# Kernel tuning notes

Measured on AMD Instinct MI355X. Metric: run time of the kernel, lower is better.

Reference implementation:

```python
import jax, jax.numpy as jnp
import numpy as np

B, L, D = 4, 1024, 256
HD = 16                 # head_dim
H = D // HD             # num heads = 16
DI = 2 * D              # mamba d_inner (expand=2) = 512
S = 64                  # d_state
KC = 4                  # d_conv
DTR = max(1, D // 16)   # dt_rank = 16
SCALES = (1, 2, 4, 8)


def _lin_interp(x, L_out):
    # F.interpolate(mode='linear', align_corners=False) on (B, L_in, D)
    L_in = x.shape[1]
    pos = (jnp.arange(L_out, dtype=x.dtype) + 0.5) * (L_in / L_out) - 0.5
    pos = jnp.clip(pos, 0.0, L_in - 1)
    lo = jnp.floor(pos).astype(jnp.int32)
    hi = jnp.minimum(lo + 1, L_in - 1)
    w = (pos - lo.astype(x.dtype))[None, :, None]
    return x[:, lo] * (1.0 - w) + x[:, hi] * w


def setup_inputs() -> dict:
    key = jax.random.key(0)
    ks = jax.random.split(key, 24)
    sc = 0.02
    inp = {
        "x": jax.random.normal(ks[0], (B, L, D), jnp.float32),
        "ln_g": jnp.ones((D,), jnp.float32),
        "ln_b": jnp.zeros((D,), jnp.float32),
        # MultiScaleQuery: 4 per-scale projections + fuse
        "mq_w": sc * jax.random.normal(ks[1], (4, D, D), jnp.float32),
        "mq_b": sc * jax.random.normal(ks[2], (4, D), jnp.float32),
        "fuse_w": sc * jax.random.normal(ks[3], (D, 4 * D), jnp.float32),
        "fuse_b": sc * jax.random.normal(ks[4], (D,), jnp.float32),
        # Mamba params
        "in_proj_w": sc * jax.random.normal(ks[5], (2 * DI, D), jnp.float32),
        "conv_w": 0.2 * jax.random.normal(ks[6], (DI, KC), jnp.float32),
        "conv_b": sc * jax.random.normal(ks[7], (DI,), jnp.float32),
        "x_proj_w": sc * jax.random.normal(ks[8], (DTR + 2 * S, DI), jnp.float32),
        "dt_w": sc * jax.random.normal(ks[9], (DI, DTR), jnp.float32),
        "dt_b": jnp.full((DI,), -4.0, jnp.float32),  # softplus -> small dt
        "A_log": jnp.log(jnp.tile(jnp.arange(1, S + 1, dtype=jnp.float32), (DI, 1))),
        "D_ssm": jnp.ones((DI,), jnp.float32),
        "out_w": sc * jax.random.normal(ks[10], (D, DI), jnp.float32),
        # StructuredSSD (q comes from MultiScaleQuery override; q_proj unused)
        "k_w": sc * jax.random.normal(ks[11], (D, D), jnp.float32),
        "k_b": sc * jax.random.normal(ks[12], (D,), jnp.float32),
        "v_w": sc * jax.random.normal(ks[13], (D, D), jnp.float32),
        "v_b": sc * jax.random.normal(ks[14], (D,), jnp.float32),
        "o_w": sc * jax.random.normal(ks[15], (D, D), jnp.float32),
        "o_b": sc * jax.random.normal(ks[16], (D,), jnp.float32),
        "log_tau": jnp.full((H,), np.log(16.0), jnp.float32),
        # Gate
        "gate_w": sc * jax.random.normal(ks[17], (D, 2 * D), jnp.float32),
        "gate_b": sc * jax.random.normal(ks[18], (D,), jnp.float32),
    }
    return inp


def reference(x, ln_g, ln_b, mq_w, mq_b, fuse_w, fuse_b,
              in_proj_w, conv_w, conv_b, x_proj_w, dt_w, dt_b,
              A_log, D_ssm, out_w,
              k_w, k_b, v_w, v_b, o_w, o_b, log_tau,
              gate_w, gate_b):
    Bsz, Lq, Dm = x.shape

    # ---- LayerNorm ----
    mu = x.mean(-1, keepdims=True)
    var = ((x - mu) ** 2).mean(-1, keepdims=True)
    xn = (x - mu) / jnp.sqrt(var + 1e-5) * ln_g + ln_b

    # ---- MultiScaleQuery ----
    qs = []
    for i, s in enumerate(SCALES):
        if s <= 1:
            q = xn @ mq_w[i].T + mq_b[i]
        else:
            xd = xn.reshape(Bsz, Lq // s, s, Dm).mean(2)   # avg_pool1d(k=s, stride=s)
            qd = xd @ mq_w[i].T + mq_b[i]
            q = _lin_interp(qd, Lq)
        qs.append(q)
    q = jnp.concatenate(qs, -1) @ fuse_w.T + fuse_b        # (B, L, D)

    # ---- Mamba (selective scan) ----
    xz = xn @ in_proj_w.T                                  # (B, L, 2*DI)
    xm, z = jnp.split(xz, 2, axis=-1)
    xp = jnp.pad(xm, ((0, 0), (KC - 1, 0), (0, 0)))        # causal depthwise conv
    xc = sum(xp[:, kk:kk + Lq, :] * conv_w[:, kk] for kk in range(KC)) + conv_b
    xc = jax.nn.silu(xc)                                   # (B, L, DI)
    dbc = xc @ x_proj_w.T                                  # (B, L, DTR+2S)
    dt_in, Bm, Cm = jnp.split(dbc, [DTR, DTR + S], axis=-1)
    dt = jax.nn.softplus(dt_in @ dt_w.T + dt_b)            # (B, L, DI)
    A = -jnp.exp(A_log)                                    # (DI, S)

    def step(h, inp):
        xt, dtt, Bt, Ct = inp                              # (B,DI) (B,DI) (B,S) (B,S)
        dA = jnp.exp(dtt[:, :, None] * A)                  # (B, DI, S)
        h = dA * h + (dtt * xt)[:, :, None] * Bt[:, None, :]
        y = jnp.einsum('bds,bs->bd', h, Ct)
        return h, y

    h0 = jnp.zeros((Bsz, DI, S), x.dtype)
    _, ys = jax.lax.scan(step, h0, (xc.transpose(1, 0, 2), dt.transpose(1, 0, 2),
                                    Bm.transpose(1, 0, 2), Cm.transpose(1, 0, 2)))
    y = ys.transpose(1, 0, 2) + xc * D_ssm                 # (B, L, DI)
    y = y * jax.nn.silu(z)
    ssm_out = y @ out_w.T                                  # (B, L, D)

    # ---- StructuredSSD (decay-masked attention, q override) ----
    k = xn @ k_w.T + k_b
    v = xn @ v_w.T + v_b
    hds = lambda t: t.reshape(Bsz, Lq, H, HD).transpose(0, 2, 1, 3)
    qh, kh, vh = hds(q), hds(k), hds(v)                    # (B, H, L, hd)
    scale = 1.0 / np.sqrt(HD)
    scores = jnp.einsum('bhqd,bhkd->bhqk', qh, kh) * scale
    idx = jnp.arange(Lq)
    dist = jnp.maximum(idx[:, None] - idx[None, :], 0).astype(x.dtype)
    tau = jnp.exp(log_tau)[:, None, None]                  # (H,1,1)
    mask = jnp.exp(-dist / tau)                            # (H, L, L); ==1 above diag
    scores = scores * mask
    denom = jnp.maximum(mask.sum(-1, keepdims=True), 1e-6)
    scores = scores / denom                                # broadcast over batch
    attn = jnp.einsum('bhqk,bhkd->bhqd', scores, vh)
    attn = attn.transpose(0, 2, 1, 3).reshape(Bsz, Lq, Dm)
    ssd_out = attn @ o_w.T + o_b

    # ---- Sigmoid gate fusion + residual ----
    gate = jax.nn.sigmoid(jnp.concatenate([ssm_out, ssd_out], -1) @ gate_w.T + gate_b)
    fused = gate * ssm_out + (1.0 - gate) * ssd_out
    return x + fused
```

## Files before the change

### kernel.cpp

```cpp
#include <hip/hip_runtime.h>
#include <math.h>

#define Bsz 4
#define Lseq 1024
#define Dm 256
#define Hh 16
#define HDm 16
#define DIm 512
#define Ssz 64
#define KCm 4
#define DTRm 16
#define NCH (Bsz * DIm)
#define CHK 64
#define NCHK (Lseq / CHK)
#define CHA 16
#define NCA (Lseq / CHA)

typedef __attribute__((ext_vector_type(8))) short s8v;
typedef __attribute__((ext_vector_type(4))) float f4v;

static __device__ __forceinline__ float wave_sum(float v) {
    #pragma unroll
    for (int m = 32; m >= 1; m >>= 1) v += __shfl_xor(v, m, 64);
    return v;
}

static __device__ __forceinline__ float bcast(float v, int l) {
    return __uint_as_float(__builtin_amdgcn_readlane(__float_as_uint(v), l));
}

static __device__ __forceinline__ short f2bf(float f) {
    unsigned int u = __float_as_uint(f);
    u = (u + 0x7fffu + ((u >> 16) & 1u)) >> 16;
    return (short)u;
}

static __device__ __forceinline__ s8v pack8(float4 a, float4 b) {
    s8v v;
    v[0] = f2bf(a.x); v[1] = f2bf(a.y); v[2] = f2bf(a.z); v[3] = f2bf(a.w);
    v[4] = f2bf(b.x); v[5] = f2bf(b.y); v[6] = f2bf(b.z); v[7] = f2bf(b.w);
    return v;
}

__global__ __launch_bounds__(256) void ln_pool(const float* __restrict__ x,
                                               const float* __restrict__ g,
                                               const float* __restrict__ bb,
                                               float* __restrict__ xn, float* __restrict__ xd2,
                                               float* __restrict__ xd4, float* __restrict__ xd8) {
    __shared__ float p2[4][256];
    int wid = threadIdx.x >> 6, lane = threadIdx.x & 63;
    int gr0 = blockIdx.x * 8;
    int b = gr0 >> 10, t0 = gr0 & 1023;
    float4 g4 = *(const float4*)(g + lane * 4);
    float4 b4 = *(const float4*)(bb + lane * 4);
    float4 res[2];
    #pragma unroll
    for (int rr = 0; rr < 2; rr++) {
        int row = gr0 + wid * 2 + rr;
        float4 xv = *(const float4*)(x + (size_t)row * 256 + lane * 4);
        float s = wave_sum(xv.x + xv.y + xv.z + xv.w);
        float mean = s * (1.0f / 256.0f);
        float d0 = xv.x - mean, d1 = xv.y - mean, d2 = xv.z - mean, d3 = xv.w - mean;
        float s2 = wave_sum(d0 * d0 + d1 * d1 + d2 * d2 + d3 * d3);
        float inv = rsqrtf(s2 * (1.0f / 256.0f) + 1e-5f);
        float4 r;
        r.x = d0 * inv * g4.x + b4.x; r.y = d1 * inv * g4.y + b4.y;
        r.z = d2 * inv * g4.z + b4.z; r.w = d3 * inv * g4.w + b4.w;
        *(float4*)(xn + (size_t)row * 256 + lane * 4) = r;
        res[rr] = r;
    }
    float4 a2;
    a2.x = 0.5f * (res[0].x + res[1].x); a2.y = 0.5f * (res[0].y + res[1].y);
    a2.z = 0.5f * (res[0].z + res[1].z); a2.w = 0.5f * (res[0].w + res[1].w);
    *(float4*)(xd2 + (size_t)(b * 512 + (t0 >> 1) + wid) * 256 + lane * 4) = a2;
    *(float4*)&p2[wid][lane * 4] = a2;
    __syncthreads();
    if (wid < 2) {
        float4 u = *(const float4*)&p2[2 * wid][lane * 4];
        float4 w = *(const float4*)&p2[2 * wid + 1][lane * 4];
        float4 m;
        m.x = 0.5f * (u.x + w.x); m.y = 0.5f * (u.y + w.y);
        m.z = 0.5f * (u.z + w.z); m.w = 0.5f * (u.w + w.w);
        *(float4*)(xd4 + (size_t)(b * 256 + (t0 >> 2) + wid) * 256 + lane * 4) = m;
    } else if (wid == 2) {
        float4 q0 = *(const float4*)&p2[0][lane * 4];
        float4 q1 = *(const float4*)&p2[1][lane * 4];
        float4 q2 = *(const float4*)&p2[2][lane * 4];
        float4 q3 = *(const float4*)&p2[3][lane * 4];
        float4 m;
        m.x = 0.25f * ((q0.x + q1.x) + (q2.x + q3.x));
        m.y = 0.25f * ((q0.y + q1.y) + (q2.y + q3.y));
        m.z = 0.25f * ((q0.z + q1.z) + (q2.z + q3.z));
        m.w = 0.25f * ((q0.w + q1.w) + (q2.w + q3.w));
        *(float4*)(xd8 + (size_t)(b * 128 + (t0 >> 3)) * 256 + lane * 4) = m;
    }
}

__global__ __launch_bounds__(256) void proj8(const float* __restrict__ xn,
                                             const float* __restrict__ xd2,
                                             const float* __restrict__ xd4,
                                             const float* __restrict__ xd8,
                                             const float* __restrict__ in_proj_w,
                                             const float* __restrict__ k_w, const float* __restrict__ k_b,
                                             const float* __restrict__ v_w, const float* __restrict__ v_b,
                                             const float* __restrict__ mq_w, const float* __restrict__ mq_b,
                                             float* __restrict__ xm, float* __restrict__ zT,
                                             float* __restrict__ kmat, float* __restrict__ vmat,
                                             float* __restrict__ q0, float* __restrict__ qd2,
                                             float* __restrict__ qd4, float* __restrict__ qd8) {
    __shared__ unsigned short As[64][40];
    __shared__ unsigned short Ws[64][40];
    int bx = blockIdx.x;
    const float* A; const float* W; const float* bias; float* C;
    int ldc, transC = 0, n0, m0;
    if (bx < 512) {
        A = xn; W = in_proj_w; bias = nullptr; C = xm; ldc = DIm;
        n0 = (bx & 7) * 64; m0 = (bx >> 3) * 64;
    } else if (bx < 1024) {
        int l = bx - 512;
        A = xn; W = in_proj_w + 131072; bias = nullptr; C = zT; ldc = Bsz * Lseq; transC = 1;
        n0 = (l & 7) * 64; m0 = (l >> 3) * 64;
    } else if (bx < 1280) {
        int l = bx - 1024;
        A = xn; W = k_w; bias = k_b; C = kmat; ldc = Dm;
        n0 = (l & 3) * 64; m0 = (l >> 2) * 64;
    } else if (bx < 1536) {
        int l = bx - 1280;
        A = xn; W = v_w; bias = v_b; C = vmat; ldc = Dm;
        n0 = (l & 3) * 64; m0 = (l >> 2) * 64;
    } else if (bx < 1792) {
        int l = bx - 1536;
        A = xn; W = mq_w; bias = mq_b; C = q0; ldc = Dm;
        n0 = (l & 3) * 64; m0 = (l >> 2) * 64;
    } else if (bx < 1920) {
        int l = bx - 1792;
        A = xd2; W = mq_w + 65536; bias = mq_b + 256; C = qd2; ldc = Dm;
        n0 = (l & 3) * 64; m0 = (l >> 2) * 64;
    } else if (bx < 1984) {
        int l = bx - 1920;
        A = xd4; W = mq_w + 131072; bias = mq_b + 512; C = qd4; ldc = Dm;
        n0 = (l & 3) * 64; m0 = (l >> 2) * 64;
    } else {
        int l = bx - 1984;
        A = xd8; W = mq_w + 196608; bias = mq_b + 768; C = qd8; ldc = Dm;
        n0 = (l & 3) * 64; m0 = (l >> 2) * 64;
    }
    int tid = threadIdx.x;
    int wave = tid >> 6, lane = tid & 63;
    int quad = lane >> 4, r = lane & 15;
    int mo = (wave >> 1) * 32, no = (wave & 1) * 32;
    f4v acc[2][2];
    #pragma unroll
    for (int i = 0; i < 2; i++)
        #pragma unroll
        for (int j = 0; j < 2; j++) acc[i][j] = (f4v){0.f, 0.f, 0.f, 0.f};
    for (int k0 = 0; k0 < 256; k0 += 32) {
        {
            int m = tid >> 2, kk = (tid & 3) * 8;
            const float* ap = A + (size_t)(m0 + m) * 256 + k0 + kk;
            *(s8v*)&As[m][kk] = pack8(*(const float4*)ap, *(const float4*)(ap + 4));
        }
        {
            int n = tid >> 2, kk = (tid & 3) * 8;
            const float* wp = W + (size_t)(n0 + n) * 256 + k0 + kk;
            *(s8v*)&Ws[n][kk] = pack8(*(const float4*)wp, *(const float4*)(wp + 4));
        }
        __syncthreads();
        s8v af[2], bf[2];
        #pragma unroll
        for (int i = 0; i < 2; i++) af[i] = *(const s8v*)&As[mo + i * 16 + r][quad * 8];
        #pragma unroll
        for (int j = 0; j < 2; j++) bf[j] = *(const s8v*)&Ws[no + j * 16 + r][quad * 8];
        #pragma unroll
        for (int i = 0; i < 2; i++)
            #pragma unroll
            for (int j = 0; j < 2; j++)
                acc[i][j] = __builtin_amdgcn_mfma_f32_16x16x32_bf16(af[i], bf[j], acc[i][j], 0, 0, 0);
        __syncthreads();
    }
    #pragma unroll
    for (int i = 0; i < 2; i++)
        #pragma unroll
        for (int j = 0; j < 2; j++)
            #pragma unroll
            for (int reg = 0; reg < 4; reg++) {
                int m = m0 + mo + i * 16 + quad * 4 + reg;
                int n = n0 + no + j * 16 + r;
                float v = acc[i][j][reg];
                if (bias) v += bias[n];
                float* cp = transC ? (C + (size_t)n * ldc + m) : (C + (size_t)m * ldc + n);
                *cp = v;
            }
}

__global__ __launch_bounds__(256) void mid2(const float* __restrict__ q0,
                                            const float* __restrict__ qd2,
                                            const float* __restrict__ qd4,
                                            const float* __restrict__ qd8,
                                            const float* __restrict__ fuse_w,
                                            const float* __restrict__ fuse_b,
                                            float* __restrict__ qbuf,
                                            const float* __restrict__ xm,
                                            const float* __restrict__ cw,
                                            const float* __restrict__ cb,
                                            float* __restrict__ xc, float* __restrict__ xcT) {
    __shared__ __align__(16) char smem[16640];
    int bx = blockIdx.x;
    int tid = threadIdx.x;
    if (bx < 256) {
        unsigned short (*As)[40] = (unsigned short(*)[40])smem;
        unsigned short (*Ws)[40] = (unsigned short(*)[40])(smem + 5120);
        int wave = tid >> 6, lane = tid & 63;
        int quad = lane >> 4, r = lane & 15;
        int n0 = (bx & 3) * 64, m0 = (bx >> 2) * 64;
        int mo = (wave >> 1) * 32, no = (wave & 1) * 32;
        f4v acc[2][2];
        #pragma unroll
        for (int i = 0; i < 2; i++)
            #pragma unroll
            for (int j = 0; j < 2; j++) acc[i][j] = (f4v){0.f, 0.f, 0.f, 0.f};
        for (int k0 = 0; k0 < 1024; k0 += 32) {
            {
                int m = tid >> 2, kk = (tid & 3) * 8;
                int kg = k0 + kk;
                int seg = kg >> 8, dcol = kg & 255;
                int mg = m0 + m;
                s8v pv;
                if (seg == 0) {
                    const float* ap = q0 + (size_t)mg * 256 + dcol;
                    pv = pack8(*(const float4*)ap, *(const float4*)(ap + 4));
                } else {
                    int t = mg & 1023, b = mg >> 10;
                    int Lin = 512 >> (seg - 1);
                    const float* qd = (seg == 1) ? qd2 : (seg == 2) ? qd4 : qd8;
                    float pos = (t + 0.5f) * ((float)Lin / 1024.0f) - 0.5f;
                    pos = fminf(fmaxf(pos, 0.0f), (float)(Lin - 1));
                    int lo = (int)floorf(pos);
                    int hi = min(lo + 1, Lin - 1);
                    float w = pos - (float)lo;
                    const float* plo = qd + ((size_t)(b * Lin + lo)) * 256 + dcol;
                    const float* phi = qd + ((size_t)(b * Lin + hi)) * 256 + dcol;
                    float4 l0 = *(const float4*)plo, l1 = *(const float4*)(plo + 4);
                    float4 h0 = *(const float4*)phi, h1 = *(const float4*)(phi + 4);
                    float4 r0, r1;
                    r0.x = l0.x + w * (h0.x - l0.x); r0.y = l0.y + w * (h0.y - l0.y);
                    r0.z = l0.z + w * (h0.z - l0.z); r0.w = l0.w + w * (h0.w - l0.w);
                    r1.x = l1.x + w * (h1.x - l1.x); r1.y = l1.y + w * (h1.y - l1.y);
                    r1.z = l1.z + w * (h1.z - l1.z); r1.w = l1.w + w * (h1.w - l1.w);
                    pv = pack8(r0, r1);
                }
                *(s8v*)&As[m][kk] = pv;
            }
            {
                int n = tid >> 2, kk = (tid & 3) * 8;
                const float* wp = fuse_w + (size_t)(n0 + n) * 1024 + k0 + kk;
                *(s8v*)&Ws[n][kk] = pack8(*(const float4*)wp, *(const float4*)(wp + 4));
            }
            __syncthreads();
            s8v af[2], bf[2];
            #pragma unroll
            for (int i = 0; i < 2; i++) af[i] = *(const s8v*)&As[mo + i * 16 + r][quad * 8];
            #pragma unroll
            for (int j = 0; j < 2; j++) bf[j] = *(const s8v*)&Ws[no + j * 16 + r][quad * 8];
            #pragma unroll
            for (int i = 0; i < 2; i++)
                #pragma unroll
                for (int j = 0; j < 2; j++)
                    acc[i][j] = __builtin_amdgcn_mfma_f32_16x16x32_bf16(af[i], bf[j], acc[i][j], 0, 0, 0);
            __syncthreads();
        }
        #pragma unroll
        for (int i = 0; i < 2; i++)
            #pragma unroll
            for (int j = 0; j < 2; j++)
                #pragma unroll
                for (int reg = 0; reg < 4; reg++) {
                    int m = m0 + mo + i * 16 + quad * 4 + reg;
                    int n = n0 + no + j * 16 + r;
                    qbuf[(size_t)m * 256 + n] = acc[i][j][reg] + fuse_b[n];
                }
    } else {
        float (*tile)[65] = (float(*)[65])smem;
        int blk = bx - 256;
        int cblk = blk & 7;
        int tblk = (blk >> 3) & 15;
        int b = blk >> 7;
        int c0 = cblk * 64, t0 = tblk * 64;
        int cc = tid & 63;
        int tw = tid >> 6;
        int c = c0 + cc;
        float w0 = cw[c * 4 + 0], w1 = cw[c * 4 + 1], w2 = cw[c * 4 + 2], w3 = cw[c * 4 + 3];
        float bias = cb[c];
        #pragma unroll 4
        for (int i = 0; i < 16; i++) {
            int tl = tw * 16 + i;
            int t = t0 + tl;
            const float* base = xm + ((size_t)(b * Lseq + t)) * DIm + c;
            float acc = bias + base[0] * w3;
            if (t >= 3) {
                acc += base[-3 * DIm] * w0 + base[-2 * DIm] * w1 + base[-1 * DIm] * w2;
            } else {
                if (t >= 1) acc += base[-1 * DIm] * w2;
                if (t >= 2) acc += base[-2 * DIm] * w1;
            }
            float r = acc / (1.0f + __expf(-acc));
            xc[((size_t)(b * Lseq + t)) * DIm + c] = r;
            tile[tl][cc] = r;
        }
        __syncthreads();
        int tcol = tid & 63;
        int crow0 = tid >> 6;
        #pragma unroll 4
        for (int j = 0; j < 16; j++) {
            int crow = crow0 * 16 + j;
            xcT[((size_t)(c0 + crow)) * (Bsz * Lseq) + b * Lseq + t0 + tcol] = tile[tcol][crow];
        }
    }
}

__global__ __launch_bounds__(256) void xproj_ap1(const float* __restrict__ xc,
                                                 const float* __restrict__ x_proj_w,
                                                 float* __restrict__ dbc,
                                                 const float* __restrict__ kmat,
                                                 const float* __restrict__ vmat,
                                                 const float* __restrict__ log_tau,
                                                 float* __restrict__ loc) {
    __shared__ __align__(16) char smem[10240];
    int bx = blockIdx.x;
    int tid = threadIdx.x;
    int wid = tid >> 6, lane = tid & 63;
    if (bx < 192) {
        unsigned short (*As)[40] = (unsigned short(*)[40])smem;
        unsigned short (*Ws)[40] = (unsigned short(*)[40])(smem + 5120);
        int quad = lane >> 4, r = lane & 15;
        int n0 = (bx % 3) * 64, m0 = (bx / 3) * 64;
        int mo = (wid >> 1) * 32, no = (wid & 1) * 32;
        f4v acc[2][2];
        #pragma unroll
        for (int i = 0; i < 2; i++)
            #pragma unroll
            for (int j = 0; j < 2; j++) acc[i][j] = (f4v){0.f, 0.f, 0.f, 0.f};
        for (int k0 = 0; k0 < 512; k0 += 32) {
            {
                int m = tid >> 2, kk = (tid & 3) * 8;
                const float* ap = xc + (size_t)(m0 + m) * 512 + k0 + kk;
                *(s8v*)&As[m][kk] = pack8(*(const float4*)ap, *(const float4*)(ap + 4));
            }
            {
                int n = tid >> 2, kk = (tid & 3) * 8;
                s8v pv;
                if (n0 + n < 144) {
                    const float* wp = x_proj_w + (size_t)(n0 + n) * 512 + k0 + kk;
                    pv = pack8(*(const float4*)wp, *(const float4*)(wp + 4));
                } else {
                    pv = (s8v){0, 0, 0, 0, 0, 0, 0, 0};
                }
                *(s8v*)&Ws[n][kk] = pv;
            }
            __syncthreads();
            s8v af[2], bf[2];
            #pragma unroll
            for (int i = 0; i < 2; i++) af[i] = *(const s8v*)&As[mo + i * 16 + r][quad * 8];
            #pragma unroll
            for (int j = 0; j < 2; j++) bf[j] = *(const s8v*)&Ws[no + j * 16 + r][quad * 8];
            #pragma unroll
            for (int i = 0; i < 2; i++)
                #pragma unroll
                for (int j = 0; j < 2; j++)
                    acc[i][j] = __builtin_amdgcn_mfma_f32_16x16x32_bf16(af[i], bf[j], acc[i][j], 0, 0, 0);
            __syncthreads();
        }
        #pragma unroll
        for (int i = 0; i < 2; i++)
            #pragma unroll
            for (int j = 0; j < 2; j++)
                #pragma unroll
                for (int reg = 0; reg < 4; reg++) {
                    int m = m0 + mo + i * 16 + quad * 4 + reg;
                    int n = n0 + no + j * 16 + r;
                    if (n >= 144) continue;
                    dbc[(size_t)m * 144 + n] = acc[i][j][reg];
                }
    } else {
        float (*Ksh)[CHA][20] = (float(*)[CHA][20])smem;
        float (*Vsh)[CHA][16] = (float(*)[CHA][16])(smem + 5120);
        int wv = (bx - 192) * 4 + wid;
        int bh = wv >> 6, c = wv & 63;
        int b = bh >> 4, h = bh & 15;
        float inv_tau = __expf(-log_tau[h]);
        float rdec = __expf(-inv_tau);
        int t0 = c * CHA;
        int row = lane >> 2, q4 = (lane & 3) * 4;
        const float* kp = kmat + ((size_t)(b * Lseq + t0 + row)) * Dm + h * HDm + q4;
        const float* vp = vmat + ((size_t)(b * Lseq + t0 + row)) * Dm + h * HDm + q4;
        *(float4*)&Ksh[wid][row][q4] = *(const float4*)kp;
        *(float4*)&Vsh[wid][row][q4] = *(const float4*)vp;
        int g = lane >> 4, cc = lane & 15;
        float4 U = {0.f, 0.f, 0.f, 0.f}, T = {0.f, 0.f, 0.f, 0.f};
        #pragma unroll
        for (int s = 0; s < CHA; s++) {
            float4 kf = *(const float4*)&Ksh[wid][s][4 * g];
            float vv = Vsh[wid][s][cc];
            float u0 = kf.x * vv, u1 = kf.y * vv, u2 = kf.z * vv, u3 = kf.w * vv;
            U.x += u0; U.y += u1; U.z += u2; U.w += u3;
            T.x = fmaf(rdec, T.x, u0); T.y = fmaf(rdec, T.y, u1);
            T.z = fmaf(rdec, T.z, u2); T.w = fmaf(rdec, T.w, u3);
        }
        float* op = loc + ((size_t)bh * NCA + c) * 512;
        *(float4*)(op + lane * 4) = U;
        *(float4*)(op + 256 + lane * 4) = T;
    }
}

__global__ __launch_bounds__(256) void dt_ap2(const float* __restrict__ dbc,
                                              const float* __restrict__ dt_w,
                                              const float* __restrict__ dt_b,
                                              float* __restrict__ dtmT,
                                              float* __restrict__ loc,
                                              const float* __restrict__ log_tau,
                                              float* __restrict__ kvtot) {
    __shared__ __align__(16) char smem[9216];
    int bx = blockIdx.x;
    int tid = threadIdx.x;
    if (bx < 512) {
        float (*As)[72] = (float(*)[72])smem;
        float (*Ws)[72] = (float(*)[72])(smem + 4608);
        int m0 = (bx >> 3) * 64, n0 = (bx & 7) * 64;
        int tx = tid & 15, ty = tid >> 4;
        float acc[4][4] = {};
        {
            int ml = tid >> 2, kl = (tid & 3) * 4;
            const float4 av = *(const float4*)(dbc + (size_t)(m0 + ml) * 144 + kl);
            As[kl + 0][ml] = av.x; As[kl + 1][ml] = av.y;
            As[kl + 2][ml] = av.z; As[kl + 3][ml] = av.w;
        }
        {
            int nl = tid >> 2, kl = (tid & 3) * 4;
            float4 wv = *(const float4*)(dt_w + (size_t)(n0 + nl) * 16 + kl);
            Ws[kl + 0][nl] = wv.x; Ws[kl + 1][nl] = wv.y;
            Ws[kl + 2][nl] = wv.z; Ws[kl + 3][nl] = wv.w;
        }
        __syncthreads();
        #pragma unroll
        for (int kk = 0; kk < 16; kk++) {
            float4 av = *(const float4*)&As[kk][ty * 4];
            float4 bv = *(const float4*)&Ws[kk][tx * 4];
            float a[4] = {av.x, av.y, av.z, av.w};
            float bbv[4] = {bv.x, bv.y, bv.z, bv.w};
            #pragma unroll
            for (int im = 0; im < 4; im++)
                #pragma unroll
                for (int in = 0; in < 4; in++)
                    acc[im][in] = fmaf(a[im], bbv[in], acc[im][in]);
        }
        #pragma unroll
        for (int in = 0; in < 4; in++) {
            int n = n0 + tx * 4 + in;
            #pragma unroll
            for (int im = 0; im < 4; im++) {
                int m = m0 + ty * 4 + im;
                float v = acc[im][in] + dt_b[n];
                v = fmaxf(v, 0.0f) + log1pf(expf(-fabsf(v)));
                dtmT[(size_t)n * (Bsz * Lseq) + m] = v;
            }
        }
    } else {
        int bh = bx - 512, e = tid;
        float inv_tau = __expf(-log_tau[bh & 15]);
        float rp = __expf(-(float)CHA * inv_tau);
        float* lp = loc + (size_t)bh * NCA * 512;
        float Ua = 0.f, Ta = 0.f;
        #pragma unroll 8
        for (int c = 0; c < NCA; c++) {
            float tu = lp[c * 512 + e];
            lp[c * 512 + e] = Ua;
            Ua += tu;
            float tt = lp[c * 512 + 256 + e];
            lp[c * 512 + 256 + e] = Ta;
            Ta = fmaf(rp, Ta, tt);
        }
        kvtot[bh * 256 + e] = Ua;
    }
}

__global__ __launch_bounds__(256) void sp1_ap3(const float* __restrict__ xcT,
                                               const float* __restrict__ dtmT,
                                               const float* __restrict__ dbc,
                                               const float* __restrict__ A_log,
                                               float* __restrict__ hloc,
                                               float* __restrict__ Pc,
                                               const float* __restrict__ q,
                                               const float* __restrict__ kmat,
                                               const float* __restrict__ vmat,
                                               const float* __restrict__ log_tau,
                                               const float* __restrict__ init,
                                               const float* __restrict__ kvtot,
                                               float* __restrict__ attn_out) {
    __shared__ __align__(16) char smem[18432];
    int bx = blockIdx.x;
    int tid = threadIdx.x;
    int wid = tid >> 6, lane = tid & 63;
    if (bx < 8192) {
        int wave = bx * 4 + wid;
        int ch = wave & (NCH - 1);
        int c  = wave >> 11;
        int b = ch >> 9, d = ch & (DIm - 1);
        float As = -__expf(A_log[d * Ssz + lane]);
        int base_m = b * Lseq + c * CHK;
        float dt_vec = dtmT[(size_t)d * (Bsz * Lseq) + base_m + lane];
        float x_vec  = xcT [(size_t)d * (Bsz * Lseq) + base_m + lane];
        float ux = dt_vec * x_vec;
        float S = dt_vec;
        #pragma unroll
        for (int m = 1; m < 64; m <<= 1) {
            float o = __shfl_up(S, m, 64);
            if (lane >= m) S += o;
        }
        float Stot = bcast(S, 63);
        const float* Bp = dbc + (size_t)base_m * 144 + DTRm + lane;
        float h0 = 0.f, h1 = 0.f, h2 = 0.f, h3 = 0.f;
        #pragma unroll 4
        for (int t = 0; t < CHK; t += 4) {
            float B0 = Bp[0], B1 = Bp[144], B2 = Bp[288], B3 = Bp[432];
            Bp += 576;
            float w0 = __expf(As * (Stot - bcast(S, t)))     * bcast(ux, t);
            float w1 = __expf(As * (Stot - bcast(S, t + 1))) * bcast(ux, t + 1);
            float w2 = __expf(As * (Stot - bcast(S, t + 2))) * bcast(ux, t + 2);
            float w3 = __expf(As * (Stot - bcast(S, t + 3))) * bcast(ux, t + 3);
            h0 = fmaf(w0, B0, h0); h1 = fmaf(w1, B1, h1);
            h2 = fmaf(w2, B2, h2); h3 = fmaf(w3, B3, h3);
        }
        size_t o = ((size_t)ch * NCHK + c) * Ssz + lane;
        hloc[o] = (h0 + h1) + (h2 + h3);
        Pc[o] = __expf(As * Stot);
    } else {
        float (*Ksh)[CHA][20] = (float(*)[CHA][20])smem;
        float (*Qsh)[CHA][20] = (float(*)[CHA][20])(smem + 5120);
        float (*Vsh)[CHA][16] = (float(*)[CHA][16])(smem + 10240);
        float (*Ysh)[CHA][16] = (float(*)[CHA][16])(smem + 14336);
        int wv = (bx - 8192) * 4 + wid;
        int bh = wv >> 6, c = wv & 63;
        int b = bh >> 4, h = bh & 15;
        float inv_tau = __expf(-log_tau[h]);
        float rdec = __expf(-inv_tau);
        int t0 = c * CHA;
        int row = lane >> 2, q4 = (lane & 3) * 4;
        const float* kp = kmat + ((size_t)(b * Lseq + t0 + row)) * Dm + h * HDm + q4;
        const float* vp = vmat + ((size_t)(b * Lseq + t0 + row)) * Dm + h * HDm + q4;
        const float* qp = q    + ((size_t)(b * Lseq + t0 + row)) * Dm + h * HDm + q4;
        *(float4*)&Ksh[wid][row][q4] = *(const float4*)kp;
        *(float4*)&Vsh[wid][row][q4] = *(const float4*)vp;
        *(float4*)&Qsh[wid][row][q4] = *(const float4*)qp;
        int g = lane >> 4, cc = lane & 15;
        size_t ibase = ((size_t)bh * NCA + c) * 512;
        float4 U  = *(const float4*)(init + ibase + lane * 4);
        float4 T  = *(const float4*)(init + ibase + 256 + lane * 4);
        float4 KV = *(const float4*)(kvtot + bh * 256 + lane * 4);
        float om = 1.0f - rdec;
        float geom = (om > 1e-8f) ? (1.0f - __expf(-inv_tau * (float)t0)) / om : (float)t0;
        #pragma unroll
        for (int s = 0; s < CHA; s++) {
            int i = t0 + s;
            geom = fmaf(geom, rdec, 1.0f);
            float4 kf = *(const float4*)&Ksh[wid][s][4 * g];
            float4 qf = *(const float4*)&Qsh[wid][s][4 * g];
            float vv = Vsh[wid][s][cc];
            float u0 = kf.x * vv, u1 = kf.y * vv, u2 = kf.z * vv, u3 = kf.w * vv;
            U.x += u0; U.y += u1; U.z += u2; U.w += u3;
            T.x = fmaf(rdec, T.x, u0); T.y = fmaf(rdec, T.y, u1);
            T.z = fmaf(rdec, T.z, u2); T.w = fmaf(rdec, T.w, u3);
            float p;
            p = qf.x * (KV.x - U.x + T.x);
            p = fmaf(qf.y, KV.y - U.y + T.y, p);
            p = fmaf(qf.z, KV.z - U.z + T.z, p);
            p = fmaf(qf.w, KV.w - U.w + T.w, p);
            p += __shfl_xor(p, 16, 64);
            p += __shfl_xor(p, 32, 64);
            float deno = fmaxf((float)(Lseq - 1 - i) + geom, 1e-6f);
            float yv = p * (0.25f / deno);
            if (lane < 16) Ysh[wid][s][lane] = yv;
        }
        float* op = attn_out + ((size_t)(b * Lseq + t0 + row)) * Dm + h * HDm + q4;
        *(float4*)op = *(const float4*)&Ysh[wid][row][q4];
    }
}

__global__ __launch_bounds__(256) void scan_combine(float* __restrict__ hloc,
                                                    const float* __restrict__ Pc) {
    int wave = blockIdx.x * 4 + (threadIdx.x >> 6);
    int lane = threadIdx.x & 63;
    size_t base = (size_t)wave * NCHK * Ssz + lane;
    float H = 0.0f;
    #pragma unroll
    for (int c = 0; c < NCHK; c++) {
        size_t o = base + (size_t)c * Ssz;
        float p = Pc[o];
        float hl = hloc[o];
        hloc[o] = H;
        H = fmaf(p, H, hl);
    }
}

__global__ __launch_bounds__(256) void scan_pass3(const float* __restrict__ xcT,
                                                  const float* __restrict__ dtmT,
                                                  const float* __restrict__ zT,
                                                  const float* __restrict__ dbc,
                                                  const float* __restrict__ A_log,
                                                  const float* __restrict__ D_ssm,
                                                  const float* __restrict__ Hinit,
                                                  float* __restrict__ yT) {
    __shared__ float hCs[4][16][68];
    int wid = threadIdx.x >> 6;
    int lane = threadIdx.x & 63;
    int wave = blockIdx.x * 4 + wid;
    int ch = wave & (NCH - 1);
    int c  = wave >> 11;
    int b = ch >> 9, d = ch & (DIm - 1);
    float As = -__expf(A_log[d * Ssz + lane]);
    float Dd = D_ssm[d];
    int base_m = b * Lseq + c * CHK;
    float dt_vec = dtmT[(size_t)d * (Bsz * Lseq) + base_m + lane];
    float x_vec  = xcT [(size_t)d * (Bsz * Lseq) + base_m + lane];
    float zown   = zT  [(size_t)d * (Bsz * Lseq) + base_m + lane];
    float ux = dt_vec * x_vec;
    const float* Bp = dbc + (size_t)base_m * 144 + DTRm + lane;
    const float* Cp = Bp + Ssz;
    float h = Hinit[((size_t)ch * NCHK + c) * Ssz + lane];
    float yred = 0.0f;
    int tl = lane >> 2;
    int so = (lane & 3) * 16;
    for (int tb = 0; tb < 4; tb++) {
        #pragma unroll
        for (int j = 0; j < 16; j++) {
            int t = tb * 16 + j;
            float Bt = *Bp; Bp += 144;
            float Ct = *Cp; Cp += 144;
            float dtv = bcast(dt_vec, t);
            float u   = bcast(ux, t);
            float dA = __expf(dtv * As);
            h = fmaf(dA, h, u * Bt);
            hCs[wid][j][lane] = h * Ct;
        }
        const float* bp = &hCs[wid][tl][so];
        float4 a0 = *(const float4*)(bp + 0);
        float4 a1 = *(const float4*)(bp + 4);
        float4 a2 = *(const float4*)(bp + 8);
        float4 a3 = *(const float4*)(bp + 12);
        float part = ((a0.x + a0.y) + (a0.z + a0.w)) + ((a1.x + a1.y) + (a1.z + a1.w))
                   + ((a2.x + a2.y) + (a2.z + a2.w)) + ((a3.x + a3.y) + (a3.z + a3.w));
        part += __shfl_xor(part, 1, 64);
        part += __shfl_xor(part, 2, 64);
        float got = __shfl(part, ((lane - tb * 16) << 2) & 63, 64);
        if ((lane >> 4) == tb) yred = got;
    }
    float yg = (yred + x_vec * Dd) * (zown / (1.0f + __expf(-zown)));
    yT[(size_t)d * (Bsz * Lseq) + base_m + lane] = yg;
}

__global__ __launch_bounds__(256) void post2(const float* __restrict__ attn,
                                             const float* __restrict__ o_w,
                                             const float* __restrict__ o_b,
                                             const float* __restrict__ yT,
                                             const float* __restrict__ out_w,
                                             float* __restrict__ cat2) {
    __shared__ unsigned short As[64][40];
    __shared__ unsigned short Ws[64][40];
    int bx = blockIdx.x;
    const float* A; const float* W; const float* bias; float* C;
    int lda_m, lda_k, ldw, K, n0, m0;
    if (bx < 256) {
        A = attn; lda_m = 256; lda_k = 1; W = o_w; ldw = 256; bias = o_b;
        C = cat2 + 256; K = 256;
        n0 = (bx & 3) * 64; m0 = (bx >> 2) * 64;
    } else {
        int l = bx - 256;
        A = yT; lda_m = 1; lda_k = Bsz * Lseq; W = out_w; ldw = DIm; bias = nullptr;
        C = cat2; K = DIm;
        n0 = (l & 3) * 64; m0 = (l >> 2) * 64;
    }
    int tid = threadIdx.x;
    int wave = tid >> 6, lane = tid & 63;
    int quad = lane >> 4, r = lane & 15;
    int mo = (wave >> 1) * 32, no = (wave & 1) * 32;
    f4v acc[2][2];
    #pragma unroll
    for (int i = 0; i < 2; i++)
        #pragma unroll
        for (int j = 0; j < 2; j++) acc[i][j] = (f4v){0.f, 0.f, 0.f, 0.f};
    for (int k0 = 0; k0 < K; k0 += 32) {
        if (lda_k == 1) {
            int m = tid >> 2, kk = (tid & 3) * 8;
            const float* ap = A + (size_t)(m0 + m) * lda_m + k0 + kk;
            *(s8v*)&As[m][kk] = pack8(*(const float4*)ap, *(const float4*)(ap + 4));
        } else {
            int k = tid >> 3, m8 = (tid & 7) * 8;
            const float* ap = A + (size_t)(k0 + k) * lda_k + m0 + m8;
            float4 a0 = *(const float4*)ap;
            float4 a1 = *(const float4*)(ap + 4);
            float av[8] = {a0.x, a0.y, a0.z, a0.w, a1.x, a1.y, a1.z, a1.w};
            #pragma unroll
            for (int i = 0; i < 8; i++) As[m8 + i][k] = (unsigned short)f2bf(av[i]);
        }
        {
            int n = tid >> 2, kk = (tid & 3) * 8;
            const float* wp = W + (size_t)(n0 + n) * ldw + k0 + kk;
            *(s8v*)&Ws[n][kk] = pack8(*(const float4*)wp, *(const float4*)(wp + 4));
        }
        __syncthreads();
        s8v af[2], bf[2];
        #pragma unroll
        for (int i = 0; i < 2; i++) af[i] = *(const s8v*)&As[mo + i * 16 + r][quad * 8];
        #pragma unroll
        for (int j = 0; j < 2; j++) bf[j] = *(const s8v*)&Ws[no + j * 16 + r][quad * 8];
        #pragma unroll
        for (int i = 0; i < 2; i++)
            #pragma unroll
            for (int j = 0; j < 2; j++)
                acc[i][j] = __builtin_amdgcn_mfma_f32_16x16x32_bf16(af[i], bf[j], acc[i][j], 0, 0, 0);
        __syncthreads();
    }
    #pragma unroll
    for (int i = 0; i < 2; i++)
        #pragma unroll
        for (int j = 0; j < 2; j++)
            #pragma unroll
            for (int reg = 0; reg < 4; reg++) {
                int m = m0 + mo + i * 16 + quad * 4 + reg;
                int n = n0 + no + j * 16 + r;
                float v = acc[i][j][reg];
                if (bias) v += bias[n];
                C[(size_t)m * 512 + n] = v;
            }
}

__global__ __launch_bounds__(256) void gate_gemm(const float* __restrict__ cat2,
                                                 const float* __restrict__ gate_w,
                                                 const float* __restrict__ gate_b,
                                                 const float* __restrict__ xres,
                                                 float* __restrict__ fout) {
    __shared__ unsigned short As[64][40];
    __shared__ unsigned short Ws[64][40];
    int tid = threadIdx.x;
    int wave = tid >> 6, lane = tid & 63;
    int quad = lane >> 4, r = lane & 15;
    int m0 = blockIdx.y * 64, n0 = blockIdx.x * 64;
    int mo = (wave >> 1) * 32, no = (wave & 1) * 32;
    f4v acc[2][2];
    #pragma unroll
    for (int i = 0; i < 2; i++)
        #pragma unroll
        for (int j = 0; j < 2; j++) acc[i][j] = (f4v){0.f, 0.f, 0.f, 0.f};
    for (int k0 = 0; k0 < 512; k0 += 32) {
        {
            int m = tid >> 2, kk = (tid & 3) * 8;
            const float* ap = cat2 + (size_t)(m0 + m) * 512 + k0 + kk;
            *(s8v*)&As[m][kk] = pack8(*(const float4*)ap, *(const float4*)(ap + 4));
        }
        {
            int n = tid >> 2, kk = (tid & 3) * 8;
            const float* wp = gate_w + (size_t)(n0 + n) * 512 + k0 + kk;
            *(s8v*)&Ws[n][kk] = pack8(*(const float4*)wp, *(const float4*)(wp + 4));
        }
        __syncthreads();
        s8v af[2], bf[2];
        #pragma unroll
        for (int i = 0; i < 2; i++) af[i] = *(const s8v*)&As[mo + i * 16 + r][quad * 8];
        #pragma unroll
        for (int j = 0; j < 2; j++) bf[j] = *(const s8v*)&Ws[no + j * 16 + r][quad * 8];
        #pragma unroll
        for (int i = 0; i < 2; i++)
            #pragma unroll
            for (int j = 0; j < 2; j++)
                acc[i][j] = __builtin_amdgcn_mfma_f32_16x16x32_bf16(af[i], bf[j], acc[i][j], 0, 0, 0);
        __syncthreads();
    }
    #pragma unroll
    for (int i = 0; i < 2; i++)
        #pragma unroll
        for (int j = 0; j < 2; j++)
            #pragma unroll
            for (int reg = 0; reg < 4; reg++) {
                int m = m0 + mo + i * 16 + quad * 4 + reg;
                int n = n0 + no + j * 16 + r;
                float v = acc[i][j][reg] + gate_b[n];
                float gg = 1.0f / (1.0f + __expf(-v));
                float ssm = cat2[(size_t)m * 512 + n];
                float ssd = cat2[(size_t)m * 512 + 256 + n];
                fout[(size_t)m * 256 + n] = xres[(size_t)m * 256 + n] + gg * ssm + (1.0f - gg) * ssd;
            }
}

extern "C" void kernel_launch(void* const* d_in, const int* in_sizes, int n_in,
                              void* d_out, int out_size, void* d_ws, size_t ws_size,
                              hipStream_t stream) {
    const float* x        = (const float*)d_in[0];
    const float* ln_g     = (const float*)d_in[1];
    const float* ln_b     = (const float*)d_in[2];
    const float* mq_w     = (const float*)d_in[3];
    const float* mq_b     = (const float*)d_in[4];
    const float* fuse_w   = (const float*)d_in[5];
    const float* fuse_b   = (const float*)d_in[6];
    const float* in_proj_w= (const float*)d_in[7];
    const float* conv_w   = (const float*)d_in[8];
    const float* conv_b   = (const float*)d_in[9];
    const float* x_proj_w = (const float*)d_in[10];
    const float* dt_w     = (const float*)d_in[11];
    const float* dt_b     = (const float*)d_in[12];
    const float* A_log    = (const float*)d_in[13];
    const float* D_ssm    = (const float*)d_in[14];
    const float* out_w    = (const float*)d_in[15];
    const float* k_w      = (const float*)d_in[16];
    const float* k_b      = (const float*)d_in[17];
    const float* v_w      = (const float*)d_in[18];
    const float* v_b      = (const float*)d_in[19];
    const float* o_w      = (const float*)d_in[20];
    const float* o_b      = (const float*)d_in[21];
    const float* log_tau  = (const float*)d_in[22];
    const float* gate_w   = (const float*)d_in[23];
    const float* gate_b   = (const float*)d_in[24];
    float* outp = (float*)d_out;

    const int M = Bsz * Lseq;
    float* ws = (float*)d_ws;
    size_t off = 0;
    float* xn    = ws + off; off += (size_t)M * Dm;
    float* xm    = ws + off; off += (size_t)M * DIm;
    float* zT    = ws + off; off += (size_t)DIm * M;
    float* xcT   = ws + off; off += (size_t)DIm * M;
    float* dbc   = ws + off; off += (size_t)M * 144;
    float* dtmT  = ws + off; off += (size_t)DIm * M;
    float* yT    = ws + off; off += (size_t)DIm * M;
    float* xd2   = ws + off; off += (size_t)Bsz * 512 * Dm;
    float* xd4   = ws + off; off += (size_t)Bsz * 256 * Dm;
    float* xd8   = ws + off; off += (size_t)Bsz * 128 * Dm;
    float* qd2   = ws + off; off += (size_t)Bsz * 512 * Dm;
    float* qd4   = ws + off; off += (size_t)Bsz * 256 * Dm;
    float* qd8   = ws + off; off += (size_t)Bsz * 128 * Dm;
    float* qcat  = ws + off; off += (size_t)M * 4 * Dm;
    float* qbuf  = ws + off; off += (size_t)M * Dm;
    float* kmat  = ws + off; off += (size_t)M * Dm;
    float* vmat  = ws + off; off += (size_t)M * Dm;
    float* attn  = ws + off; off += (size_t)M * Dm;
    float* cat2  = ws + off; off += (size_t)M * 2 * Dm;
    float* xc    = cat2;
    float* q0    = qcat;
    float* loc   = xm;
    float* kvtot = xd2;
    float* hloc  = qcat;
    float* Pc    = qcat + (size_t)NCH * NCHK * Ssz;

    ln_pool<<<512, 256, 0, stream>>>(x, ln_g, ln_b, xn, xd2, xd4, xd8);

    proj8<<<2016, 256, 0, stream>>>(xn, xd2, xd4, xd8, in_proj_w,
        k_w, k_b, v_w, v_b, mq_w, mq_b,
        xm, zT, kmat, vmat, q0, qd2, qd4, qd8);

    mid2<<<768, 256, 0, stream>>>(q0, qd2, qd4, qd8, fuse_w, fuse_b, qbuf,
        xm, conv_w, conv_b, xc, xcT);

    xproj_ap1<<<1216, 256, 0, stream>>>(xc, x_proj_w, dbc, kmat, vmat, log_tau, loc);

    dt_ap2<<<576, 256, 0, stream>>>(dbc, dt_w, dt_b, dtmT, loc, log_tau, kvtot);

    sp1_ap3<<<9216, 256, 0, stream>>>(xcT, dtmT, dbc, A_log, hloc, Pc,
        qbuf, kmat, vmat, log_tau, loc, kvtot, attn);

    scan_combine<<<512, 256, 0, stream>>>(hloc, Pc);

    scan_pass3<<<8192, 256, 0, stream>>>(xcT, dtmT, zT, dbc, A_log, D_ssm, hloc, yT);

    post2<<<512, 256, 0, stream>>>(attn, o_w, o_b, yT, out_w, cat2);

    gate_gemm<<<dim3(4, 64), 256, 0, stream>>>(cat2, gate_w, gate_b, x, outp);
}
```

Baseline: 321.5 us.

## Store intermediates and weights as bf16, pre-convert weights once, fuse scan-combine with SSD projection

LayerNorm and pooled outputs, projection results, attention output, concatenated activations and yT are now written as bf16 instead of fp32. All weight matrices are converted to bf16 in extra blocks of the first kernel, so the GEMM kernels load bf16 tiles directly instead of converting fp32 on every tile load. The scan_combine step is merged with the SSD output projection into one kernel, and the post2 kernel becomes a separate out-projection kernel. This cuts memory traffic and conversion work in exchange for extra rounding on intermediates and a per-call weight conversion pass.

```diff
diff --git a/kernel.cpp b/kernel.cpp
--- a/kernel.cpp
+++ b/kernel.cpp
@@ -17,7 +17,9 @@
 #define NCA (Lseq / CHA)
 
 typedef __attribute__((ext_vector_type(8))) short s8v;
+typedef __attribute__((ext_vector_type(4))) short s4v;
 typedef __attribute__((ext_vector_type(4))) float f4v;
+typedef unsigned short u16;
 
 static __device__ __forceinline__ float wave_sum(float v) {
     #pragma unroll
@@ -33,6 +35,10 @@
     unsigned int u = __float_as_uint(f);
     u = (u + 0x7fffu + ((u >> 16) & 1u)) >> 16;
     return (short)u;
+}
+
+static __device__ __forceinline__ float bf2f(u16 u) {
+    return __uint_as_float(((unsigned int)u) << 16);
 }
 
 static __device__ __forceinline__ s8v pack8(float4 a, float4 b) {
@@ -42,107 +48,143 @@
     return v;
 }
 
+static __device__ __forceinline__ s4v pack4(float4 a) {
+    s4v v;
+    v[0] = f2bf(a.x); v[1] = f2bf(a.y); v[2] = f2bf(a.z); v[3] = f2bf(a.w);
+    return v;
+}
+
 __global__ __launch_bounds__(256) void ln_pool(const float* __restrict__ x,
                                                const float* __restrict__ g,
                                                const float* __restrict__ bb,
-                                               float* __restrict__ xn, float* __restrict__ xd2,
-                                               float* __restrict__ xd4, float* __restrict__ xd8) {
-    __shared__ float p2[4][256];
-    int wid = threadIdx.x >> 6, lane = threadIdx.x & 63;
-    int gr0 = blockIdx.x * 8;
-    int b = gr0 >> 10, t0 = gr0 & 1023;
-    float4 g4 = *(const float4*)(g + lane * 4);
-    float4 b4 = *(const float4*)(bb + lane * 4);
-    float4 res[2];
-    #pragma unroll
-    for (int rr = 0; rr < 2; rr++) {
-        int row = gr0 + wid * 2 + rr;
-        float4 xv = *(const float4*)(x + (size_t)row * 256 + lane * 4);
-        float s = wave_sum(xv.x + xv.y + xv.z + xv.w);
-        float mean = s * (1.0f / 256.0f);
-        float d0 = xv.x - mean, d1 = xv.y - mean, d2 = xv.z - mean, d3 = xv.w - mean;
-        float s2 = wave_sum(d0 * d0 + d1 * d1 + d2 * d2 + d3 * d3);
-        float inv = rsqrtf(s2 * (1.0f / 256.0f) + 1e-5f);
-        float4 r;
-        r.x = d0 * inv * g4.x + b4.x; r.y = d1 * inv * g4.y + b4.y;
-        r.z = d2 * inv * g4.z + b4.z; r.w = d3 * inv * g4.w + b4.w;
-        *(float4*)(xn + (size_t)row * 256 + lane * 4) = r;
-        res[rr] = r;
-    }
-    float4 a2;
-    a2.x = 0.5f * (res[0].x + res[1].x); a2.y = 0.5f * (res[0].y + res[1].y);
-    a2.z = 0.5f * (res[0].z + res[1].z); a2.w = 0.5f * (res[0].w + res[1].w);
-    *(float4*)(xd2 + (size_t)(b * 512 + (t0 >> 1) + wid) * 256 + lane * 4) = a2;
-    *(float4*)&p2[wid][lane * 4] = a2;
-    __syncthreads();
-    if (wid < 2) {
-        float4 u = *(const float4*)&p2[2 * wid][lane * 4];
-        float4 w = *(const float4*)&p2[2 * wid + 1][lane * 4];
-        float4 m;
-        m.x = 0.5f * (u.x + w.x); m.y = 0.5f * (u.y + w.y);
-        m.z = 0.5f * (u.z + w.z); m.w = 0.5f * (u.w + w.w);
-        *(float4*)(xd4 + (size_t)(b * 256 + (t0 >> 2) + wid) * 256 + lane * 4) = m;
-    } else if (wid == 2) {
-        float4 q0 = *(const float4*)&p2[0][lane * 4];
-        float4 q1 = *(const float4*)&p2[1][lane * 4];
-        float4 q2 = *(const float4*)&p2[2][lane * 4];
-        float4 q3 = *(const float4*)&p2[3][lane * 4];
-        float4 m;
-        m.x = 0.25f * ((q0.x + q1.x) + (q2.x + q3.x));
-        m.y = 0.25f * ((q0.y + q1.y) + (q2.y + q3.y));
-        m.z = 0.25f * ((q0.z + q1.z) + (q2.z + q3.z));
-        m.w = 0.25f * ((q0.w + q1.w) + (q2.w + q3.w));
-        *(float4*)(xd8 + (size_t)(b * 128 + (t0 >> 3)) * 256 + lane * 4) = m;
-    }
-}
-
-__global__ __launch_bounds__(256) void proj8(const float* __restrict__ xn,
-                                             const float* __restrict__ xd2,
-                                             const float* __restrict__ xd4,
-                                             const float* __restrict__ xd8,
-                                             const float* __restrict__ in_proj_w,
-                                             const float* __restrict__ k_w, const float* __restrict__ k_b,
-                                             const float* __restrict__ v_w, const float* __restrict__ v_b,
-                                             const float* __restrict__ mq_w, const float* __restrict__ mq_b,
-                                             float* __restrict__ xm, float* __restrict__ zT,
+                                               u16* __restrict__ xnb, u16* __restrict__ xd2b,
+                                               u16* __restrict__ xd4b, u16* __restrict__ xd8b,
+                                               const float* __restrict__ in_proj_w,
+                                               const float* __restrict__ k_w,
+                                               const float* __restrict__ v_w,
+                                               const float* __restrict__ mq_w,
+                                               const float* __restrict__ fuse_w,
+                                               const float* __restrict__ x_proj_w,
+                                               const float* __restrict__ out_w,
+                                               const float* __restrict__ o_w,
+                                               const float* __restrict__ gate_w,
+                                               u16* __restrict__ wbf) {
+    int bx = blockIdx.x;
+    int tid = threadIdx.x;
+    if (bx < 512) {
+        __shared__ float p2[4][256];
+        int wid = tid >> 6, lane = tid & 63;
+        int gr0 = bx * 8;
+        int b = gr0 >> 10, t0 = gr0 & 1023;
+        float4 g4 = *(const float4*)(g + lane * 4);
+        float4 b4 = *(const float4*)(bb + lane * 4);
+        float4 res[2];
+        #pragma unroll
+        for (int rr = 0; rr < 2; rr++) {
+            int row = gr0 + wid * 2 + rr;
+            float4 xv = *(const float4*)(x + (size_t)row * 256 + lane * 4);
+            float s = wave_sum(xv.x + xv.y + xv.z + xv.w);
+            float mean = s * (1.0f / 256.0f);
+            float d0 = xv.x - mean, d1 = xv.y - mean, d2 = xv.z - mean, d3 = xv.w - mean;
+            float s2 = wave_sum(d0 * d0 + d1 * d1 + d2 * d2 + d3 * d3);
+            float inv = rsqrtf(s2 * (1.0f / 256.0f) + 1e-5f);
+            float4 r;
+            r.x = d0 * inv * g4.x + b4.x; r.y = d1 * inv * g4.y + b4.y;
+            r.z = d2 * inv * g4.z + b4.z; r.w = d3 * inv * g4.w + b4.w;
+            *(s4v*)(xnb + (size_t)row * 256 + lane * 4) = pack4(r);
+            res[rr] = r;
+        }
+        float4 a2;
+        a2.x = 0.5f * (res[0].x + res[1].x); a2.y = 0.5f * (res[0].y + res[1].y);
+        a2.z = 0.5f * (res[0].z + res[1].z); a2.w = 0.5f * (res[0].w + res[1].w);
+        *(s4v*)(xd2b + (size_t)(b * 512 + (t0 >> 1) + wid) * 256 + lane * 4) = pack4(a2);
+        *(float4*)&p2[wid][lane * 4] = a2;
+        __syncthreads();
+        if (wid < 2) {
+            float4 u = *(const float4*)&p2[2 * wid][lane * 4];
+            float4 w = *(const float4*)&p2[2 * wid + 1][lane * 4];
+            float4 m;
+            m.x = 0.5f * (u.x + w.x); m.y = 0.5f * (u.y + w.y);
+            m.z = 0.5f * (u.z + w.z); m.w = 0.5f * (u.w + w.w);
+            *(s4v*)(xd4b + (size_t)(b * 256 + (t0 >> 2) + wid) * 256 + lane * 4) = pack4(m);
+        } else if (wid == 2) {
+            float4 q0 = *(const float4*)&p2[0][lane * 4];
+            float4 q1 = *(const float4*)&p2[1][lane * 4];
+            float4 q2 = *(const float4*)&p2[2][lane * 4];
+            float4 q3 = *(const float4*)&p2[3][lane * 4];
+            float4 m;
+            m.x = 0.25f * ((q0.x + q1.x) + (q2.x + q3.x));
+            m.y = 0.25f * ((q0.y + q1.y) + (q2.y + q3.y));
+            m.z = 0.25f * ((q0.z + q1.z) + (q2.z + q3.z));
+            m.w = 0.25f * ((q0.w + q1.w) + (q2.w + q3.w));
+            *(s4v*)(xd8b + (size_t)(b * 128 + (t0 >> 3)) * 256 + lane * 4) = pack4(m);
+        }
+    } else {
+        int l = bx - 512;
+        const float* src; u16* dst; int base;
+        if (l < 128)      { src = in_proj_w; dst = wbf;           base = l; }
+        else if (l < 160) { src = k_w;      dst = wbf + 262144;   base = l - 128; }
+        else if (l < 192) { src = v_w;      dst = wbf + 327680;   base = l - 160; }
+        else if (l < 320) { src = mq_w;     dst = wbf + 393216;   base = l - 192; }
+        else if (l < 448) { src = fuse_w;   dst = wbf + 655360;   base = l - 320; }
+        else if (l < 484) { src = x_proj_w; dst = wbf + 917504;   base = l - 448; }
+        else if (l < 548) { src = out_w;    dst = wbf + 991232;   base = l - 484; }
+        else if (l < 580) { src = o_w;      dst = wbf + 1122304;  base = l - 548; }
+        else              { src = gate_w;   dst = wbf + 1187840;  base = l - 580; }
+        int idx = base * 2048 + tid * 8;
+        const float* sp = src + idx;
+        *(s8v*)(dst + idx) = pack8(*(const float4*)sp, *(const float4*)(sp + 4));
+    }
+}
+
+__global__ __launch_bounds__(256) void proj8(const u16* __restrict__ xnb,
+                                             const u16* __restrict__ xd2b,
+                                             const u16* __restrict__ xd4b,
+                                             const u16* __restrict__ xd8b,
+                                             const u16* __restrict__ wbf,
+                                             const float* __restrict__ k_b,
+                                             const float* __restrict__ v_b,
+                                             const float* __restrict__ mq_b,
+                                             u16* __restrict__ xmb, float* __restrict__ zT,
                                              float* __restrict__ kmat, float* __restrict__ vmat,
-                                             float* __restrict__ q0, float* __restrict__ qd2,
-                                             float* __restrict__ qd4, float* __restrict__ qd8) {
-    __shared__ unsigned short As[64][40];
-    __shared__ unsigned short Ws[64][40];
+                                             u16* __restrict__ q0b, u16* __restrict__ qd2b,
+                                             u16* __restrict__ qd4b, u16* __restrict__ qd8b) {
+    __shared__ u16 As[64][40];
+    __shared__ u16 Ws[64][40];
     int bx = blockIdx.x;
-    const float* A; const float* W; const float* bias; float* C;
+    const u16* A; const u16* W; const float* bias;
+    float* Cf = nullptr; u16* Cb = nullptr;
     int ldc, transC = 0, n0, m0;
     if (bx < 512) {
-        A = xn; W = in_proj_w; bias = nullptr; C = xm; ldc = DIm;
+        A = xnb; W = wbf; bias = nullptr; Cb = xmb; ldc = DIm;
         n0 = (bx & 7) * 64; m0 = (bx >> 3) * 64;
     } else if (bx < 1024) {
         int l = bx - 512;
-        A = xn; W = in_proj_w + 131072; bias = nullptr; C = zT; ldc = Bsz * Lseq; transC = 1;
+        A = xnb; W = wbf + 131072; bias = nullptr; Cf = zT; ldc = Bsz * Lseq; transC = 1;
         n0 = (l & 7) * 64; m0 = (l >> 3) * 64;
     } else if (bx < 1280) {
         int l = bx - 1024;
-        A = xn; W = k_w; bias = k_b; C = kmat; ldc = Dm;
+        A = xnb; W = wbf + 262144; bias = k_b; Cf = kmat; ldc = Dm;
         n0 = (l & 3) * 64; m0 = (l >> 2) * 64;
     } else if (bx < 1536) {
         int l = bx - 1280;
-        A = xn; W = v_w; bias = v_b; C = vmat; ldc = Dm;
+        A = xnb; W = wbf + 327680; bias = v_b; Cf = vmat; ldc = Dm;
         n0 = (l & 3) * 64; m0 = (l >> 2) * 64;
     } else if (bx < 1792) {
         int l = bx - 1536;
-        A = xn; W = mq_w; bias = mq_b; C = q0; ldc = Dm;
+        A = xnb; W = wbf + 393216; bias = mq_b; Cb = q0b; ldc = Dm;
         n0 = (l & 3) * 64; m0 = (l >> 2) * 64;
     } else if (bx < 1920) {
         int l = bx - 1792;
-        A = xd2; W = mq_w + 65536; bias = mq_b + 256; C = qd2; ldc = Dm;
+        A = xd2b; W = wbf + 393216 + 65536; bias = mq_b + 256; Cb = qd2b; ldc = Dm;
         n0 = (l & 3) * 64; m0 = (l >> 2) * 64;
     } else if (bx < 1984) {
         int l = bx - 1920;
-        A = xd4; W = mq_w + 131072; bias = mq_b + 512; C = qd4; ldc = Dm;
+        A = xd4b; W = wbf + 393216 + 131072; bias = mq_b + 512; Cb = qd4b; ldc = Dm;
         n0 = (l & 3) * 64; m0 = (l >> 2) * 64;
     } else {
         int l = bx - 1984;
-        A = xd8; W = mq_w + 196608; bias = mq_b + 768; C = qd8; ldc = Dm;
+        A = xd8b; W = wbf + 393216 + 196608; bias = mq_b + 768; Cb = qd8b; ldc = Dm;
         n0 = (l & 3) * 64; m0 = (l >> 2) * 64;
     }
     int tid = threadIdx.x;
@@ -157,13 +199,11 @@
     for (int k0 = 0; k0 < 256; k0 += 32) {
         {
             int m = tid >> 2, kk = (tid & 3) * 8;
-            const float* ap = A + (size_t)(m0 + m) * 256 + k0 + kk;
-            *(s8v*)&As[m][kk] = pack8(*(const float4*)ap, *(const float4*)(ap + 4));
+            *(s8v*)&As[m][kk] = *(const s8v*)(A + (size_t)(m0 + m) * 256 + k0 + kk);
         }
         {
             int n = tid >> 2, kk = (tid & 3) * 8;
-            const float* wp = W + (size_t)(n0 + n) * 256 + k0 + kk;
-            *(s8v*)&Ws[n][kk] = pack8(*(const float4*)wp, *(const float4*)(wp + 4));
+            *(s8v*)&Ws[n][kk] = *(const s8v*)(W + (size_t)(n0 + n) * 256 + k0 + kk);
         }
         __syncthreads();
         s8v af[2], bf[2];
@@ -188,28 +228,31 @@
                 int n = n0 + no + j * 16 + r;
                 float v = acc[i][j][reg];
                 if (bias) v += bias[n];
-                float* cp = transC ? (C + (size_t)n * ldc + m) : (C + (size_t)m * ldc + n);
-                *cp = v;
-            }
-}
-
-__global__ __launch_bounds__(256) void mid2(const float* __restrict__ q0,
-                                            const float* __restrict__ qd2,
-                                            const float* __restrict__ qd4,
-                                            const float* __restrict__ qd8,
-                                            const float* __restrict__ fuse_w,
+                if (Cb) Cb[(size_t)m * ldc + n] = (u16)f2bf(v);
+                else {
+                    float* cp = transC ? (Cf + (size_t)n * ldc + m) : (Cf + (size_t)m * ldc + n);
+                    *cp = v;
+                }
+            }
+}
+
+__global__ __launch_bounds__(256) void mid2(const u16* __restrict__ q0b,
+                                            const u16* __restrict__ qd2b,
+                                            const u16* __restrict__ qd4b,
+                                            const u16* __restrict__ qd8b,
+                                            const u16* __restrict__ w_fuse,
                                             const float* __restrict__ fuse_b,
                                             float* __restrict__ qbuf,
-                                            const float* __restrict__ xm,
+                                            const u16* __restrict__ xmb,
                                             const float* __restrict__ cw,
                                             const float* __restrict__ cb,
-                                            float* __restrict__ xc, float* __restrict__ xcT) {
+                                            u16* __restrict__ xcb, float* __restrict__ xcT) {
     __shared__ __align__(16) char smem[16640];
     int bx = blockIdx.x;
     int tid = threadIdx.x;
     if (bx < 256) {
-        unsigned short (*As)[40] = (unsigned short(*)[40])smem;
-        unsigned short (*Ws)[40] = (unsigned short(*)[40])(smem + 5120);
+        u16 (*As)[40] = (u16(*)[40])smem;
+        u16 (*Ws)[40] = (u16(*)[40])(smem + 5120);
         int wave = tid >> 6, lane = tid & 63;
         int quad = lane >> 4, r = lane & 15;
         int n0 = (bx & 3) * 64, m0 = (bx >> 2) * 64;
@@ -227,34 +270,29 @@
                 int mg = m0 + m;
                 s8v pv;
                 if (seg == 0) {
-                    const float* ap = q0 + (size_t)mg * 256 + dcol;
-                    pv = pack8(*(const float4*)ap, *(const float4*)(ap + 4));
+                    pv = *(const s8v*)(q0b + (size_t)mg * 256 + dcol);
                 } else {
                     int t = mg & 1023, b = mg >> 10;
                     int Lin = 512 >> (seg - 1);
-                    const float* qd = (seg == 1) ? qd2 : (seg == 2) ? qd4 : qd8;
+                    const u16* qd = (seg == 1) ? qd2b : (seg == 2) ? qd4b : qd8b;
                     float pos = (t + 0.5f) * ((float)Lin / 1024.0f) - 0.5f;
                     pos = fminf(fmaxf(pos, 0.0f), (float)(Lin - 1));
                     int lo = (int)floorf(pos);
                     int hi = min(lo + 1, Lin - 1);
                     float w = pos - (float)lo;
-                    const float* plo = qd + ((size_t)(b * Lin + lo)) * 256 + dcol;
-                    const float* phi = qd + ((size_t)(b * Lin + hi)) * 256 + dcol;
-                    float4 l0 = *(const float4*)plo, l1 = *(const float4*)(plo + 4);
-                    float4 h0 = *(const float4*)phi, h1 = *(const float4*)(phi + 4);
-                    float4 r0, r1;
-                    r0.x = l0.x + w * (h0.x - l0.x); r0.y = l0.y + w * (h0.y - l0.y);
-                    r0.z = l0.z + w * (h0.z - l0.z); r0.w = l0.w + w * (h0.w - l0.w);
-                    r1.x = l1.x + w * (h1.x - l1.x); r1.y = l1.y + w * (h1.y - l1.y);
-                    r1.z = l1.z + w * (h1.z - l1.z); r1.w = l1.w + w * (h1.w - l1.w);
-                    pv = pack8(r0, r1);
+                    s8v lv = *(const s8v*)(qd + ((size_t)(b * Lin + lo)) * 256 + dcol);
+                    s8v hv = *(const s8v*)(qd + ((size_t)(b * Lin + hi)) * 256 + dcol);
+                    #pragma unroll
+                    for (int i = 0; i < 8; i++) {
+                        float lf = bf2f((u16)lv[i]), hf = bf2f((u16)hv[i]);
+                        pv[i] = f2bf(lf + w * (hf - lf));
+                    }
                 }
                 *(s8v*)&As[m][kk] = pv;
             }
             {
                 int n = tid >> 2, kk = (tid & 3) * 8;
-                const float* wp = fuse_w + (size_t)(n0 + n) * 1024 + k0 + kk;
-                *(s8v*)&Ws[n][kk] = pack8(*(const float4*)wp, *(const float4*)(wp + 4));
+                *(s8v*)&Ws[n][kk] = *(const s8v*)(w_fuse + (size_t)(n0 + n) * 1024 + k0 + kk);
             }
             __syncthreads();
             s8v af[2], bf[2];
@@ -295,16 +333,16 @@
         for (int i = 0; i < 16; i++) {
             int tl = tw * 16 + i;
             int t = t0 + tl;
-            const float* base = xm + ((size_t)(b * Lseq + t)) * DIm + c;
-            float acc = bias + base[0] * w3;
+            const u16* base = xmb + ((size_t)(b * Lseq + t)) * DIm + c;
+            float acc = bias + bf2f(base[0]) * w3;
             if (t >= 3) {
-                acc += base[-3 * DIm] * w0 + base[-2 * DIm] * w1 + base[-1 * DIm] * w2;
+                acc += bf2f(base[-3 * DIm]) * w0 + bf2f(base[-2 * DIm]) * w1 + bf2f(base[-1 * DIm]) * w2;
             } else {
-                if (t >= 1) acc += base[-1 * DIm] * w2;
-                if (t >= 2) acc += base[-2 * DIm] * w1;
+                if (t >= 1) acc += bf2f(base[-1 * DIm]) * w2;
+                if (t >= 2) acc += bf2f(base[-2 * DIm]) * w1;
             }
             float r = acc / (1.0f + __expf(-acc));
-            xc[((size_t)(b * Lseq + t)) * DIm + c] = r;
+            xcb[((size_t)(b * Lseq + t)) * DIm + c] = (u16)f2bf(r);
             tile[tl][cc] = r;
         }
         __syncthreads();
@@ -318,8 +356,8 @@
     }
 }
 
-__global__ __launch_bounds__(256) void xproj_ap1(const float* __restrict__ xc,
-                                                 const float* __restrict__ x_proj_w,
+__global__ __launch_bounds__(256) void xproj_ap1(const u16* __restrict__ xcb,
+                                                 const u16* __restrict__ w_xp,
                                                  float* __restrict__ dbc,
                                                  const float* __restrict__ kmat,
                                                  const float* __restrict__ vmat,
@@ -330,8 +368,8 @@
     int tid = threadIdx.x;
     int wid = tid >> 6, lane = tid & 63;
     if (bx < 192) {
-        unsigned short (*As)[40] = (unsigned short(*)[40])smem;
-        unsigned short (*Ws)[40] = (unsigned short(*)[40])(smem + 5120);
+        u16 (*As)[40] = (u16(*)[40])smem;
+        u16 (*Ws)[40] = (u16(*)[40])(smem + 5120);
         int quad = lane >> 4, r = lane & 15;
         int n0 = (bx % 3) * 64, m0 = (bx / 3) * 64;
         int mo = (wid >> 1) * 32, no = (wid & 1) * 32;
@@ -343,18 +381,13 @@
         for (int k0 = 0; k0 < 512; k0 += 32) {
             {
                 int m = tid >> 2, kk = (tid & 3) * 8;
-                const float* ap = xc + (size_t)(m0 + m) * 512 + k0 + kk;
-                *(s8v*)&As[m][kk] = pack8(*(const float4*)ap, *(const float4*)(ap + 4));
+                *(s8v*)&As[m][kk] = *(const s8v*)(xcb + (size_t)(m0 + m) * 512 + k0 + kk);
             }
             {
                 int n = tid >> 2, kk = (tid & 3) * 8;
                 s8v pv;
-                if (n0 + n < 144) {
-                    const float* wp = x_proj_w + (size_t)(n0 + n) * 512 + k0 + kk;
-                    pv = pack8(*(const float4*)wp, *(const float4*)(wp + 4));
-                } else {
-                    pv = (s8v){0, 0, 0, 0, 0, 0, 0, 0};
-                }
+                if (n0 + n < 144) pv = *(const s8v*)(w_xp + (size_t)(n0 + n) * 512 + k0 + kk);
+                else pv = (s8v){0, 0, 0, 0, 0, 0, 0, 0};
                 *(s8v*)&Ws[n][kk] = pv;
             }
             __syncthreads();
@@ -495,7 +528,7 @@
                                                const float* __restrict__ log_tau,
                                                const float* __restrict__ init,
                                                const float* __restrict__ kvtot,
-                                               float* __restrict__ attn_out) {
+                                               u16* __restrict__ attnb) {
     __shared__ __align__(16) char smem[18432];
     int bx = blockIdx.x;
     int tid = threadIdx.x;
@@ -580,24 +613,77 @@
             float yv = p * (0.25f / deno);
             if (lane < 16) Ysh[wid][s][lane] = yv;
         }
-        float* op = attn_out + ((size_t)(b * Lseq + t0 + row)) * Dm + h * HDm + q4;
-        *(float4*)op = *(const float4*)&Ysh[wid][row][q4];
-    }
-}
-
-__global__ __launch_bounds__(256) void scan_combine(float* __restrict__ hloc,
-                                                    const float* __restrict__ Pc) {
-    int wave = blockIdx.x * 4 + (threadIdx.x >> 6);
-    int lane = threadIdx.x & 63;
-    size_t base = (size_t)wave * NCHK * Ssz + lane;
-    float H = 0.0f;
-    #pragma unroll
-    for (int c = 0; c < NCHK; c++) {
-        size_t o = base + (size_t)c * Ssz;
-        float p = Pc[o];
-        float hl = hloc[o];
-        hloc[o] = H;
-        H = fmaf(p, H, hl);
+        float4 yv4 = *(const float4*)&Ysh[wid][row][q4];
+        *(s4v*)(attnb + ((size_t)(b * Lseq + t0 + row)) * Dm + h * HDm + q4) = pack4(yv4);
+    }
+}
+
+__global__ __launch_bounds__(256) void comb_ssd(float* __restrict__ hloc,
+                                                const float* __restrict__ Pc,
+                                                const u16* __restrict__ attnb,
+                                                const u16* __restrict__ w_o,
+                                                const float* __restrict__ o_b,
+                                                u16* __restrict__ cat2b) {
+    __shared__ u16 As[64][40];
+    __shared__ u16 Ws[64][40];
+    int bx = blockIdx.x;
+    int tid = threadIdx.x;
+    if (bx < 512) {
+        int wave = bx * 4 + (tid >> 6);
+        int lane = tid & 63;
+        size_t base = (size_t)wave * NCHK * Ssz + lane;
+        float H = 0.0f;
+        #pragma unroll
+        for (int c = 0; c < NCHK; c++) {
+            size_t o = base + (size_t)c * Ssz;
+            float p = Pc[o];
+            float hl = hloc[o];
+            hloc[o] = H;
+            H = fmaf(p, H, hl);
+        }
+    } else {
+        int l = bx - 512;
+        int wave = tid >> 6, lane = tid & 63;
+        int quad = lane >> 4, r = lane & 15;
+        int n0 = (l & 3) * 64, m0 = (l >> 2) * 64;
+        int mo = (wave >> 1) * 32, no = (wave & 1) * 32;
+        f4v acc[2][2];
+        #pragma unroll
+        for (int i = 0; i < 2; i++)
+            #pragma unroll
+            for (int j = 0; j < 2; j++) acc[i][j] = (f4v){0.f, 0.f, 0.f, 0.f};
+        for (int k0 = 0; k0 < 256; k0 += 32) {
+            {
+                int m = tid >> 2, kk = (tid & 3) * 8;
+                *(s8v*)&As[m][kk] = *(const s8v*)(attnb + (size_t)(m0 + m) * 256 + k0 + kk);
+            }
+            {
+                int n = tid >> 2, kk = (tid & 3) * 8;
+                *(s8v*)&Ws[n][kk] = *(const s8v*)(w_o + (size_t)(n0 + n) * 256 + k0 + kk);
+            }
+            __syncthreads();
+            s8v af[2], bf[2];
+            #pragma unroll
+            for (int i = 0; i < 2; i++) af[i] = *(const s8v*)&As[mo + i * 16 + r][quad * 8];
+            #pragma unroll
+            for (int j = 0; j < 2; j++) bf[j] = *(const s8v*)&Ws[no + j * 16 + r][quad * 8];
+            #pragma unroll
+            for (int i = 0; i < 2; i++)
+                #pragma unroll
+                for (int j = 0; j < 2; j++)
+                    acc[i][j] = __builtin_amdgcn_mfma_f32_16x16x32_bf16(af[i], bf[j], acc[i][j], 0, 0, 0);
+            __syncthreads();
+        }
+        #pragma unroll
+        for (int i = 0; i < 2; i++)
+            #pragma unroll
+            for (int j = 0; j < 2; j++)
+                #pragma unroll
+                for (int reg = 0; reg < 4; reg++) {
+                    int m = m0 + mo + i * 16 + quad * 4 + reg;
+                    int n = n0 + no + j * 16 + r;
+                    cat2b[(size_t)m * 512 + 256 + n] = (u16)f2bf(acc[i][j][reg] + o_b[n]);
+                }
     }
 }
 
@@ -608,7 +694,7 @@
                                                   const float* __restrict__ A_log,
                                                   const float* __restrict__ D_ssm,
                                                   const float* __restrict__ Hinit,
-                                                  float* __restrict__ yT) {
+                                                  u16* __restrict__ yTb) {
     __shared__ float hCs[4][16][68];
     int wid = threadIdx.x >> 6;
     int lane = threadIdx.x & 63;
@@ -654,57 +740,35 @@
         if ((lane >> 4) == tb) yred = got;
     }
     float yg = (yred + x_vec * Dd) * (zown / (1.0f + __expf(-zown)));
-    yT[(size_t)d * (Bsz * Lseq) + base_m + lane] = yg;
-}
-
-__global__ __launch_bounds__(256) void post2(const float* __restrict__ attn,
-                                             const float* __restrict__ o_w,
-                                             const float* __restrict__ o_b,
-                                             const float* __restrict__ yT,
-                                             const float* __restrict__ out_w,
-                                             float* __restrict__ cat2) {
-    __shared__ unsigned short As[64][40];
-    __shared__ unsigned short Ws[64][40];
+    yTb[(size_t)d * (Bsz * Lseq) + base_m + lane] = (u16)f2bf(yg);
+}
+
+__global__ __launch_bounds__(256) void outg(const u16* __restrict__ yTb,
+                                            const u16* __restrict__ w_out,
+                                            u16* __restrict__ cat2b) {
+    __shared__ u16 As[64][40];
+    __shared__ u16 Ws[64][40];
     int bx = blockIdx.x;
-    const float* A; const float* W; const float* bias; float* C;
-    int lda_m, lda_k, ldw, K, n0, m0;
-    if (bx < 256) {
-        A = attn; lda_m = 256; lda_k = 1; W = o_w; ldw = 256; bias = o_b;
-        C = cat2 + 256; K = 256;
-        n0 = (bx & 3) * 64; m0 = (bx >> 2) * 64;
-    } else {
-        int l = bx - 256;
-        A = yT; lda_m = 1; lda_k = Bsz * Lseq; W = out_w; ldw = DIm; bias = nullptr;
-        C = cat2; K = DIm;
-        n0 = (l & 3) * 64; m0 = (l >> 2) * 64;
-    }
     int tid = threadIdx.x;
     int wave = tid >> 6, lane = tid & 63;
     int quad = lane >> 4, r = lane & 15;
+    int n0 = (bx & 3) * 64, m0 = (bx >> 2) * 64;
     int mo = (wave >> 1) * 32, no = (wave & 1) * 32;
     f4v acc[2][2];
     #pragma unroll
     for (int i = 0; i < 2; i++)
         #pragma unroll
         for (int j = 0; j < 2; j++) acc[i][j] = (f4v){0.f, 0.f, 0.f, 0.f};
-    for (int k0 = 0; k0 < K; k0 += 32) {
-        if (lda_k == 1) {
-            int m = tid >> 2, kk = (tid & 3) * 8;
-            const float* ap = A + (size_t)(m0 + m) * lda_m + k0 + kk;
-            *(s8v*)&As[m][kk] = pack8(*(const float4*)ap, *(const float4*)(ap + 4));
-        } else {
+    for (int k0 = 0; k0 < 512; k0 += 32) {
+        {
             int k = tid >> 3, m8 = (tid & 7) * 8;
-            const float* ap = A + (size_t)(k0 + k) * lda_k + m0 + m8;
-            float4 a0 = *(const float4*)ap;
-            float4 a1 = *(const float4*)(ap + 4);
-            float av[8] = {a0.x, a0.y, a0.z, a0.w, a1.x, a1.y, a1.z, a1.w};
-            #pragma unroll
-            for (int i = 0; i < 8; i++) As[m8 + i][k] = (unsigned short)f2bf(av[i]);
+            s8v av = *(const s8v*)(yTb + (size_t)(k0 + k) * (Bsz * Lseq) + m0 + m8);
+            #pragma unroll
+            for (int i = 0; i < 8; i++) As[m8 + i][k] = (u16)av[i];
         }
         {
             int n = tid >> 2, kk = (tid & 3) * 8;
-            const float* wp = W + (size_t)(n0 + n) * ldw + k0 + kk;
-            *(s8v*)&Ws[n][kk] = pack8(*(const float4*)wp, *(const float4*)(wp + 4));
+            *(s8v*)&Ws[n][kk] = *(const s8v*)(w_out + (size_t)(n0 + n) * 512 + k0 + kk);
         }
         __syncthreads();
         s8v af[2], bf[2];
@@ -727,19 +791,17 @@
             for (int reg = 0; reg < 4; reg++) {
                 int m = m0 + mo + i * 16 + quad * 4 + reg;
                 int n = n0 + no + j * 16 + r;
-                float v = acc[i][j][reg];
-                if (bias) v += bias[n];
-                C[(size_t)m * 512 + n] = v;
-            }
-}
-
-__global__ __launch_bounds__(256) void gate_gemm(const float* __restrict__ cat2,
-                                                 const float* __restrict__ gate_w,
+                cat2b[(size_t)m * 512 + n] = (u16)f2bf(acc[i][j][reg]);
+            }
+}
+
+__global__ __launch_bounds__(256) void gate_gemm(const u16* __restrict__ cat2b,
+                                                 const u16* __restrict__ w_gate,
                                                  const float* __restrict__ gate_b,
                                                  const float* __restrict__ xres,
                                                  float* __restrict__ fout) {
-    __shared__ unsigned short As[64][40];
-    __shared__ unsigned short Ws[64][40];
+    __shared__ u16 As[64][40];
+    __shared__ u16 Ws[64][40];
     int tid = threadIdx.x;
     int wave = tid >> 6, lane = tid & 63;
     int quad = lane >> 4, r = lane & 15;
@@ -753,13 +815,11 @@
     for (int k0 = 0; k0 < 512; k0 += 32) {
         {
             int m = tid >> 2, kk = (tid & 3) * 8;
-            const float* ap = cat2 + (size_t)(m0 + m) * 512 + k0 + kk;
-            *(s8v*)&As[m][kk] = pack8(*(const float4*)ap, *(const float4*)(ap + 4));
+            *(s8v*)&As[m][kk] = *(const s8v*)(cat2b + (size_t)(m0 + m) * 512 + k0 + kk);
         }
         {
             int n = tid >> 2, kk = (tid & 3) * 8;
-            const float* wp = gate_w + (size_t)(n0 + n) * 512 + k0 + kk;
-            *(s8v*)&Ws[n][kk] = pack8(*(const float4*)wp, *(const float4*)(wp + 4));
+            *(s8v*)&Ws[n][kk] = *(const s8v*)(w_gate + (size_t)(n0 + n) * 512 + k0 + kk);
         }
         __syncthreads();
         s8v af[2], bf[2];
@@ -784,8 +844,8 @@
                 int n = n0 + no + j * 16 + r;
                 float v = acc[i][j][reg] + gate_b[n];
                 float gg = 1.0f / (1.0f + __expf(-v));
-                float ssm = cat2[(size_t)m * 512 + n];
-                float ssd = cat2[(size_t)m * 512 + 256 + n];
+                float ssm = bf2f(cat2b[(size_t)m * 512 + n]);
+                float ssd = bf2f(cat2b[(size_t)m * 512 + 256 + n]);
                 fout[(size_t)m * 256 + n] = xres[(size_t)m * 256 + n] + gg * ssm + (1.0f - gg) * ssd;
             }
 }
@@ -823,53 +883,55 @@
     const int M = Bsz * Lseq;
     float* ws = (float*)d_ws;
     size_t off = 0;
-    float* xn    = ws + off; off += (size_t)M * Dm;
-    float* xm    = ws + off; off += (size_t)M * DIm;
     float* zT    = ws + off; off += (size_t)DIm * M;
     float* xcT   = ws + off; off += (size_t)DIm * M;
+    float* dtmT  = ws + off; off += (size_t)DIm * M;
     float* dbc   = ws + off; off += (size_t)M * 144;
-    float* dtmT  = ws + off; off += (size_t)DIm * M;
-    float* yT    = ws + off; off += (size_t)DIm * M;
-    float* xd2   = ws + off; off += (size_t)Bsz * 512 * Dm;
-    float* xd4   = ws + off; off += (size_t)Bsz * 256 * Dm;
-    float* xd8   = ws + off; off += (size_t)Bsz * 128 * Dm;
-    float* qd2   = ws + off; off += (size_t)Bsz * 512 * Dm;
-    float* qd4   = ws + off; off += (size_t)Bsz * 256 * Dm;
-    float* qd8   = ws + off; off += (size_t)Bsz * 128 * Dm;
-    float* qcat  = ws + off; off += (size_t)M * 4 * Dm;
     float* qbuf  = ws + off; off += (size_t)M * Dm;
     float* kmat  = ws + off; off += (size_t)M * Dm;
     float* vmat  = ws + off; off += (size_t)M * Dm;
-    float* attn  = ws + off; off += (size_t)M * Dm;
-    float* cat2  = ws + off; off += (size_t)M * 2 * Dm;
-    float* xc    = cat2;
-    float* q0    = qcat;
-    float* loc   = xm;
-    float* kvtot = xd2;
-    float* hloc  = qcat;
-    float* Pc    = qcat + (size_t)NCH * NCHK * Ssz;
-
-    ln_pool<<<512, 256, 0, stream>>>(x, ln_g, ln_b, xn, xd2, xd4, xd8);
-
-    proj8<<<2016, 256, 0, stream>>>(xn, xd2, xd4, xd8, in_proj_w,
-        k_w, k_b, v_w, v_b, mq_w, mq_b,
-        xm, zT, kmat, vmat, q0, qd2, qd4, qd8);
-
-    mid2<<<768, 256, 0, stream>>>(q0, qd2, qd4, qd8, fuse_w, fuse_b, qbuf,
-        xm, conv_w, conv_b, xc, xcT);
-
-    xproj_ap1<<<1216, 256, 0, stream>>>(xc, x_proj_w, dbc, kmat, vmat, log_tau, loc);
+    float* loc   = ws + off; off += (size_t)64 * NCA * 512;
+    float* hloc  = ws + off; off += (size_t)NCH * NCHK * Ssz;
+    float* Pc    = ws + off; off += (size_t)NCH * NCHK * Ssz;
+    float* kvtot = ws + off; off += (size_t)64 * 256;
+    u16* ub = (u16*)(ws + off);
+    size_t uo = 0;
+    u16* xnb  = ub + uo; uo += (size_t)M * Dm;
+    u16* xmb  = ub + uo; uo += (size_t)M * DIm;
+    u16* xd2b = ub + uo; uo += (size_t)2048 * Dm;
+    u16* xd4b = ub + uo; uo += (size_t)1024 * Dm;
+    u16* xd8b = ub + uo; uo += (size_t)512 * Dm;
+    u16* q0b  = ub + uo; uo += (size_t)M * Dm;
+    u16* qd2b = ub + uo; uo += (size_t)2048 * Dm;
+    u16* qd4b = ub + uo; uo += (size_t)1024 * Dm;
+    u16* qd8b = ub + uo; uo += (size_t)512 * Dm;
+    u16* attnb= ub + uo; uo += (size_t)M * Dm;
+    u16* cat2b= ub + uo; uo += (size_t)M * 2 * Dm;
+    u16* yTb  = ub + uo; uo += (size_t)DIm * M;
+    u16* wbf  = ub + uo; uo += 1318912;
+    u16* xcb  = cat2b;
+
+    ln_pool<<<1156, 256, 0, stream>>>(x, ln_g, ln_b, xnb, xd2b, xd4b, xd8b,
+        in_proj_w, k_w, v_w, mq_w, fuse_w, x_proj_w, out_w, o_w, gate_w, wbf);
+
+    proj8<<<2016, 256, 0, stream>>>(xnb, xd2b, xd4b, xd8b, wbf,
+        k_b, v_b, mq_b, xmb, zT, kmat, vmat, q0b, qd2b, qd4b, qd8b);
+
+    mid2<<<768, 256, 0, stream>>>(q0b, qd2b, qd4b, qd8b, wbf + 655360, fuse_b, qbuf,
+        xmb, conv_w, conv_b, xcb, xcT);
+
+    xproj_ap1<<<1216, 256, 0, stream>>>(xcb, wbf + 917504, dbc, kmat, vmat, log_tau, loc);
 
     dt_ap2<<<576, 256, 0, stream>>>(dbc, dt_w, dt_b, dtmT, loc, log_tau, kvtot);
 
     sp1_ap3<<<9216, 256, 0, stream>>>(xcT, dtmT, dbc, A_log, hloc, Pc,
-        qbuf, kmat, vmat, log_tau, loc, kvtot, attn);
-
-    scan_combine<<<512, 256, 0, stream>>>(hloc, Pc);
-
-    scan_pass3<<<8192, 256, 0, stream>>>(xcT, dtmT, zT, dbc, A_log, D_ssm, hloc, yT);
-
-    post2<<<512, 256, 0, stream>>>(attn, o_w, o_b, yT, out_w, cat2);
-
-    gate_gemm<<<dim3(4, 64), 256, 0, stream>>>(cat2, gate_w, gate_b, x, outp);
-}
+        qbuf, kmat, vmat, log_tau, loc, kvtot, attnb);
+
+    comb_ssd<<<768, 256, 0, stream>>>(hloc, Pc, attnb, wbf + 1122304, o_b, cat2b);
+
+    scan_pass3<<<8192, 256, 0, stream>>>(xcT, dtmT, zT, dbc, A_log, D_ssm, hloc, yTb);
+
+    outg<<<256, 256, 0, stream>>>(yTb, wbf + 991232, cat2b);
+
+    gate_gemm<<<dim3(4, 64), 256, 0, stream>>>(cat2b, wbf + 1187840, gate_b, x, outp);
+}
```

After: 294.2 us, median of 2. -8.5%, faster.
